# Kernel tuning notes

Hardware: AMD Instinct MI355X
Metric: run time of the kernel (lower is better)

Reference implementation:

```python
import jax, jax.numpy as jnp
import numpy as np

B, S, D, H, DFF = 4, 2048, 1024, 16, 4096
DK = D // H


def layer_norm(x, g, b, eps=1e-5):
    mu = jnp.mean(x, axis=-1, keepdims=True)
    var = jnp.mean((x - mu) ** 2, axis=-1, keepdims=True)
    return (x - mu) / jnp.sqrt(var + eps) * g + b


def setup_inputs() -> dict:
    key = jax.random.key(0)
    ks = jax.random.split(key, 16)
    w = lambda k, shape: jax.random.normal(k, shape, jnp.float32) * 0.02
    return {
        "x": jax.random.normal(ks[0], (B, S, D), jnp.float32),
        "w_q": w(ks[1], (D, D)), "b_q": jnp.zeros((D,), jnp.float32),
        "w_k": w(ks[2], (D, D)), "b_k": jnp.zeros((D,), jnp.float32),
        "w_v": w(ks[3], (D, D)), "b_v": jnp.zeros((D,), jnp.float32),
        "w_o": w(ks[4], (D, D)), "b_o": jnp.zeros((D,), jnp.float32),
        "w_g": w(ks[5], (D, H)), "b_g": jnp.zeros((H,), jnp.float32),
        "w1": w(ks[6], (D, DFF)), "b1": jnp.zeros((DFF,), jnp.float32),
        "w2": w(ks[7], (DFF, D)), "b2": jnp.zeros((D,), jnp.float32),
        "g1": jnp.ones((D,), jnp.float32), "beta1": jnp.zeros((D,), jnp.float32),
        "g2": jnp.ones((D,), jnp.float32), "beta2": jnp.zeros((D,), jnp.float32),
        "mask": jnp.ones((B, 1, 1, S), jnp.int32),
    }


def reference(x, w_q, b_q, w_k, b_k, w_v, b_v, w_o, b_o, w_g, b_g,
              w1, b1, w2, b2, g1, beta1, g2, beta2, mask):
    b, s, d = x.shape
    scale = DK ** -0.5
    # QKV projections -> [B,H,S,DK]
    q = (x @ w_q + b_q).reshape(b, s, H, DK).transpose(0, 2, 1, 3)
    k = (x @ w_k + b_k).reshape(b, s, H, DK).transpose(0, 2, 1, 3)
    v = (x @ w_v + b_v).reshape(b, s, H, DK).transpose(0, 2, 1, 3)
    scores = jnp.einsum("bhqd,bhkd->bhqk", q, k) * scale  # [B,H,S,S]
    scores = jnp.where(mask == 0, jnp.float32(-1e9), scores)
    attn = jax.nn.softmax(scores, axis=-1)
    # per-(token, head) sigmoid gate applied post-softmax
    gate = jax.nn.sigmoid(x @ w_g + b_g)            # [B,S,H]
    attn = attn * gate.transpose(0, 2, 1)[..., None]  # [B,H,S,1]
    ctx = jnp.einsum("bhqk,bhkd->bhqd", attn, v)
    ctx = ctx.transpose(0, 2, 1, 3).reshape(b, s, d)
    attn_out = ctx @ w_o + b_o
    x1 = layer_norm(x + attn_out, g1, beta1)
    ff = jax.nn.gelu(x1 @ w1 + b1, approximate=False) @ w2 + b2
    return layer_norm(x1 + ff, g2, beta2)
```

## Files before the change

kernel.cpp:

```cpp
#include <hip/hip_runtime.h>
#include <hip/hip_bf16.h>
#include <cstdint>


typedef __bf16 bf16x8 __attribute__((ext_vector_type(8)));
typedef float  f32x4  __attribute__((ext_vector_type(4)));

__device__ __forceinline__ uint16_t f2bf_bits(float f) {
    __hip_bfloat16 h = __float2bfloat16(f);
    return __builtin_bit_cast(uint16_t, h);
}

#define GLOAD16(ldsb, gp) __builtin_amdgcn_global_load_lds( \
    (const __attribute__((address_space(1))) void*)(gp),    \
    (__attribute__((address_space(3))) void*)(ldsb), 16, 0, 0)

__global__ __launch_bounds__(256) void cast_bf16_kernel(
    const float* __restrict__ in, __hip_bfloat16* __restrict__ out, size_t n4)
{
    size_t i = (size_t)blockIdx.x * blockDim.x + threadIdx.x;
    if (i >= n4) return;
    float4 v = ((const float4*)in)[i];
    ushort4 o;
    o.x = f2bf_bits(v.x); o.y = f2bf_bits(v.y);
    o.z = f2bf_bits(v.z); o.w = f2bf_bits(v.w);
    ((ushort4*)out)[i] = o;
}

__global__ __launch_bounds__(256) void transpose_cast_kernel(
    const float* __restrict__ in, __hip_bfloat16* __restrict__ out, int K, int N)
{
    __shared__ float t[32][33];
    int n0 = blockIdx.x * 32, k0 = blockIdx.y * 32;
    int tx = threadIdx.x, ty = threadIdx.y;
#pragma unroll
    for (int i = 0; i < 4; ++i)
        t[ty + i * 8][tx] = in[(size_t)(k0 + ty + i * 8) * N + n0 + tx];
    __syncthreads();
#pragma unroll
    for (int i = 0; i < 4; ++i)
        out[(size_t)(n0 + ty + i * 8) * K + k0 + tx] = __float2bfloat16(t[tx][ty + i * 8]);
}

__global__ __launch_bounds__(256) void gate_kernel(
    const float* __restrict__ x, const float* __restrict__ wg,
    const float* __restrict__ bg, float* __restrict__ gate)
{
    int tid = threadIdx.x, lane = tid & 63, wid = tid >> 6;
    int row = blockIdx.x * 4 + wid;
    const float* xr = x + (size_t)row * 1024;
    float acc[16];
#pragma unroll
    for (int hh = 0; hh < 16; ++hh) acc[hh] = 0.0f;
    for (int k = lane; k < 1024; k += 64) {
        float xv = xr[k];
        const float* wr = wg + (size_t)k * 16;
#pragma unroll
        for (int hh = 0; hh < 16; ++hh) acc[hh] = fmaf(xv, wr[hh], acc[hh]);
    }
#pragma unroll
    for (int hh = 0; hh < 16; ++hh) {
#pragma unroll
        for (int d = 1; d < 64; d <<= 1) acc[hh] += __shfl_xor(acc[hh], d);
    }
    if (lane < 16) {
        float v = 0.0f;
#pragma unroll
        for (int hh = 0; hh < 16; ++hh)
            if (lane == hh) v = acc[hh] + bg[hh];
        gate[(size_t)row * 16 + lane] = 1.0f / (1.0f + __expf(-v));
    }
}

__global__ __launch_bounds__(256) void ln_kernel(
    const float* __restrict__ A, const float* __restrict__ Bx,
    const float* __restrict__ g, const float* __restrict__ beta,
    float* __restrict__ outf, __hip_bfloat16* __restrict__ outb)
{
    int row = blockIdx.x, tid = threadIdx.x;
    const float4* a4 = (const float4*)(A  + (size_t)row * 1024);
    const float4* b4 = (const float4*)(Bx + (size_t)row * 1024);
    float4 va = a4[tid], vb = b4[tid];
    float x0 = va.x + vb.x, x1 = va.y + vb.y, x2 = va.z + vb.z, x3 = va.w + vb.w;
    float s  = x0 + x1 + x2 + x3;
    float sq = x0 * x0 + x1 * x1 + x2 * x2 + x3 * x3;
#pragma unroll
    for (int d = 1; d < 64; d <<= 1) { s += __shfl_xor(s, d); sq += __shfl_xor(sq, d); }
    __shared__ float ss[4], ssq[4];
    int wid = tid >> 6, lane = tid & 63;
    if (lane == 0) { ss[wid] = s; ssq[wid] = sq; }
    __syncthreads();
    s  = ss[0] + ss[1] + ss[2] + ss[3];
    sq = ssq[0] + ssq[1] + ssq[2] + ssq[3];
    float mean = s * (1.0f / 1024.0f);
    float var  = sq * (1.0f / 1024.0f) - mean * mean;
    float rstd = rsqrtf(var + 1e-5f);
    float4 gv = ((const float4*)g)[tid], bv = ((const float4*)beta)[tid];
    float y0 = (x0 - mean) * rstd * gv.x + bv.x;
    float y1 = (x1 - mean) * rstd * gv.y + bv.y;
    float y2 = (x2 - mean) * rstd * gv.z + bv.z;
    float y3 = (x3 - mean) * rstd * gv.w + bv.w;
    float4 o; o.x = y0; o.y = y1; o.z = y2; o.w = y3;
    ((float4*)(outf + (size_t)row * 1024))[tid] = o;
    if (outb) {
        ushort4 ob;
        ob.x = f2bf_bits(y0); ob.y = f2bf_bits(y1);
        ob.z = f2bf_bits(y2); ob.w = f2bf_bits(y3);
        ((ushort4*)(outb + (size_t)row * 1024))[tid] = ob;
    }
}

template<int EPI>
__global__ __launch_bounds__(256, 2) void gemm128(
    const __hip_bfloat16* __restrict__ A,
    const __hip_bfloat16* __restrict__ BT,
    const float* __restrict__ bias,
    void* __restrict__ Cout, int M, int N, int K)
{
    __shared__ __align__(16) __hip_bfloat16 As[128 * 64];
    __shared__ __align__(16) __hip_bfloat16 Bs[128 * 64];
    const int tid = threadIdx.x, lane = tid & 63, wid = tid >> 6;
    const int bx = blockIdx.x, by = blockIdx.y;
    const int wr = wid >> 1, wc = wid & 1;

    f32x4 acc[4][4];
#pragma unroll
    for (int i = 0; i < 4; ++i)
#pragma unroll
        for (int j = 0; j < 4; ++j) acc[i][j] = (f32x4){0.f, 0.f, 0.f, 0.f};

    const char* Abase = (const char*)A  + (size_t)(by * 128) * K * 2;
    const char* Bbase = (const char*)BT + (size_t)(bx * 128) * K * 2;
    char* AsB = (char*)As; char* BsB = (char*)Bs;
    const int laneRow = lane >> 3;
    const int laneCol = (lane & 7) * 16;

    for (int ks = 0; ks < K; ks += 64) {
#pragma unroll
        for (int j = 0; j < 4; ++j) {
            int r = j * 32 + wid * 8 + laneRow;
            size_t goff = (size_t)r * K * 2 + (size_t)ks * 2 + laneCol;
            GLOAD16(AsB + j * 4096 + wid * 1024, Abase + goff);
            GLOAD16(BsB + j * 4096 + wid * 1024, Bbase + goff);
        }
        __syncthreads();
#pragma unroll
        for (int kk = 0; kk < 2; ++kk) {
            const int kob = (kk * 32 + (lane >> 4) * 8) * 2;
            bf16x8 a[4], b[4];
#pragma unroll
            for (int mt = 0; mt < 4; ++mt)
                a[mt] = *(const bf16x8*)(AsB + (wr * 64 + mt * 16 + (lane & 15)) * 128 + kob);
#pragma unroll
            for (int nt = 0; nt < 4; ++nt)
                b[nt] = *(const bf16x8*)(BsB + (wc * 64 + nt * 16 + (lane & 15)) * 128 + kob);
#pragma unroll
            for (int mt = 0; mt < 4; ++mt)
#pragma unroll
                for (int nt = 0; nt < 4; ++nt)
                    acc[mt][nt] = __builtin_amdgcn_mfma_f32_16x16x32_bf16(
                        a[mt], b[nt], acc[mt][nt], 0, 0, 0);
        }
        __syncthreads();
    }

    const int m0 = by * 128 + wr * 64;
    const int n0 = bx * 128 + wc * 64;
#pragma unroll
    for (int mt = 0; mt < 4; ++mt) {
#pragma unroll
        for (int nt = 0; nt < 4; ++nt) {
            int n = n0 + nt * 16 + (lane & 15);
            float bv = bias[n];
#pragma unroll
            for (int j = 0; j < 4; ++j) {
                int m = m0 + mt * 16 + (lane >> 4) * 4 + j;
                float v = acc[mt][nt][j] + bv;
                ((float*)Cout)[(size_t)m * N + n] = v;
            }
        }
    }
}

template<int EPI>
__global__ __launch_bounds__(512, 2) void gemm256(
    const __hip_bfloat16* __restrict__ A,
    const __hip_bfloat16* __restrict__ BT,
    const float* __restrict__ bias0,
    const float* __restrict__ bias1,
    const float* __restrict__ bias2,
    __hip_bfloat16* __restrict__ out0,
    __hip_bfloat16* __restrict__ out1,
    __hip_bfloat16* __restrict__ out2,
    int M, int N, int K)
{
    __shared__ __align__(16) char lds_[131072];
    const int tid = threadIdx.x;
    const int lane = tid & 63;
    const int l15 = lane & 15;
    const int wid = tid >> 6;
    const int wm = wid >> 2, wn = wid & 3;

    const int NBX = N >> 8;
    const int cpx = ((M >> 8) * NBX) >> 3;
    const int nl = ((int)blockIdx.x & 7) * cpx + ((int)blockIdx.x >> 3);
    const int by = nl / NBX, bx = nl % NBX;

    const char* Abase = (const char*)A  + (size_t)(by * 256) * K * 2;
    const char* Bbase = (const char*)BT + (size_t)(bx * 256) * K * 2;

    const int srow = tid >> 3;
    const int ssw  = ((tid & 7) ^ (srow & 7)) * 16;

    f32x4 acc[8][4];
#pragma unroll
    for (int i = 0; i < 8; ++i)
#pragma unroll
        for (int j = 0; j < 4; ++j) acc[i][j] = (f32x4){0.f, 0.f, 0.f, 0.f};

    auto stageA = [&](int d, int c, int ks) {
        const char* src = Abase + ((size_t)(c * 64 + srow) * K + ks) * 2 + ssw;
        GLOAD16(lds_ + d * 65536 + c * 8192 + wid * 1024, src);
    };
    auto stageB = [&](int d, int c, int ks) {
        const char* src = Bbase + ((size_t)(c * 64 + srow) * K + ks) * 2 + ssw;
        GLOAD16(lds_ + d * 65536 + 32768 + c * 8192 + wid * 1024, src);
    };

    const int NT = K >> 6;
    stageB(0, 0, 0); stageB(0, 1, 0); stageB(0, 2, 0); stageB(0, 3, 0);
    stageA(0, 0, 0); stageA(0, 2, 0); stageA(0, 1, 0); stageA(0, 3, 0);
    asm volatile("s_waitcnt vmcnt(0)" ::: "memory");
    __builtin_amdgcn_s_barrier();

    for (int t = 0; t < NT; ++t) {
        const int cur = t & 1, nxt = cur ^ 1;
        const int ksn = (t + 1) << 6;
        const bool st = (t + 1 < NT);
        const char* ldsA = lds_ + cur * 65536;
        const char* ldsB = ldsA + 32768;

        bf16x8 bfr[4][2];
#pragma unroll
        for (int p = 0; p < 4; ++p) {
            if (p == 0) {
#pragma unroll
                for (int nf = 0; nf < 4; ++nf) {
                    const int br = wn * 64 + nf * 16 + l15;
#pragma unroll
                    for (int kk = 0; kk < 2; ++kk) {
                        const int kb = kk * 64 + (lane >> 4) * 16;
                        bfr[nf][kk] = *(const bf16x8*)(ldsB + (br >> 6) * 8192 +
                            (br & 63) * 128 + (kb ^ ((br & 7) << 4)));
                    }
                }
            }
            bf16x8 afr[2][2];
#pragma unroll
            for (int mi = 0; mi < 2; ++mi) {
                const int ar = wm * 128 + (2 * p + mi) * 16 + l15;
#pragma unroll
                for (int kk = 0; kk < 2; ++kk) {
                    const int kb = kk * 64 + (lane >> 4) * 16;
                    afr[mi][kk] = *(const bf16x8*)(ldsA + (ar >> 6) * 8192 +
                        (ar & 63) * 128 + (kb ^ ((ar & 7) << 4)));
                }
            }
            if (st) {
                if      (p == 0) { stageB(nxt, 0, ksn); stageB(nxt, 1, ksn); }
                else if (p == 1) { stageB(nxt, 2, ksn); stageB(nxt, 3, ksn); }
                else if (p == 2) { stageA(nxt, 0, ksn); stageA(nxt, 2, ksn); }
                else             { stageA(nxt, 1, ksn); stageA(nxt, 3, ksn); }
            }
            __builtin_amdgcn_s_barrier();
            __builtin_amdgcn_s_setprio(1);
#pragma unroll
            for (int mi = 0; mi < 2; ++mi)
#pragma unroll
                for (int nf = 0; nf < 4; ++nf)
#pragma unroll
                    for (int kk = 0; kk < 2; ++kk)
                        acc[2 * p + mi][nf] = __builtin_amdgcn_mfma_f32_16x16x32_bf16(
                            afr[mi][kk], bfr[nf][kk], acc[2 * p + mi][nf], 0, 0, 0);
            __builtin_amdgcn_s_setprio(0);
            if (p == 1) asm volatile("s_waitcnt vmcnt(4)" ::: "memory");
            if (p == 3) asm volatile("s_waitcnt vmcnt(2)" ::: "memory");
            __builtin_amdgcn_s_barrier();
        }
    }

    const int nbase = bx * 256 + wn * 64;
    const int mbase = by * 256 + wm * 128;
    if constexpr (EPI == 5) {
        const int reg = nbase >> 10;
        const float* bias = (reg == 0) ? bias0 : (reg == 1) ? bias1 : bias2;
#pragma unroll
        for (int mf = 0; mf < 8; ++mf) {
#pragma unroll
            for (int nf = 0; nf < 4; ++nf) {
                const int n = nbase + nf * 16 + l15;
                const int nn = n & 1023, h = nn >> 6, dk = nn & 63;
                const float bv = bias[nn];
#pragma unroll
                for (int j = 0; j < 4; ++j) {
                    const int m = mbase + mf * 16 + (lane >> 4) * 4 + j;
                    const int b = m >> 11, s = m & 2047;
                    const float v = acc[mf][nf][j] + bv;
                    if (reg == 0)
                        out0[((((size_t)b * 16 + h) * 2048 + s) << 6) + dk] =
                            __float2bfloat16(v * 0.125f);
                    else if (reg == 1)
                        out1[((((size_t)b * 16 + h) * 2048 + s) << 6) + dk] =
                            __float2bfloat16(v);
                    else
                        out2[(((size_t)b * 16 + h) * 64 + dk) * 2048 + s] =
                            __float2bfloat16(v);
                }
            }
        }
    } else {
#pragma unroll
        for (int mf = 0; mf < 8; ++mf) {
#pragma unroll
            for (int nf = 0; nf < 4; ++nf) {
                const int n = nbase + nf * 16 + l15;
                const float bv = bias0[n];
#pragma unroll
                for (int j = 0; j < 4; ++j) {
                    const int m = mbase + mf * 16 + (lane >> 4) * 4 + j;
                    const float v = acc[mf][nf][j] + bv;
                    const float ge = 0.5f * v * (1.0f + erff(v * 0.70710678118654752f));
                    out0[(size_t)m * N + n] = __float2bfloat16(ge);
                }
            }
        }
    }
}

__global__ __launch_bounds__(256, 2) void attn_kernel(
    const __hip_bfloat16* __restrict__ Q,
    const __hip_bfloat16* __restrict__ Kg,
    const __hip_bfloat16* __restrict__ Vt,
    const float* __restrict__ gate,
    const int* __restrict__ mask,
    __hip_bfloat16* __restrict__ ctx)
{
    __shared__ __align__(16) __hip_bfloat16 Ks[64 * 64];
    __shared__ __align__(16) __hip_bfloat16 Vs[64 * 64];
    __shared__ __align__(16) __hip_bfloat16 Ps[4][16 * 64];
    const int tid = threadIdx.x, lane = tid & 63, wid = tid >> 6;

    int lin = blockIdx.x;
    int nl  = (lin & 7) * 256 + (lin >> 3);
    const int bh = nl >> 5, qt = nl & 31;
    const int b = bh >> 4, h = bh & 15;
    const int q0 = qt * 64 + wid * 16;

    bf16x8 aq[2];
    const __hip_bfloat16* Qbase = Q + ((size_t)bh * 2048 + q0) * 64;
#pragma unroll
    for (int kk = 0; kk < 2; ++kk)
        aq[kk] = *(const bf16x8*)(Qbase + (lane & 15) * 64 + kk * 32 + (lane >> 4) * 8);

    f32x4 octx[4];
#pragma unroll
    for (int dt = 0; dt < 4; ++dt) octx[dt] = (f32x4){0.f, 0.f, 0.f, 0.f};
    float m_run[4], l_run[4];
#pragma unroll
    for (int r = 0; r < 4; ++r) { m_run[r] = -1e30f; l_run[r] = 0.0f; }

    const char* Kbase = (const char*)(Kg + (size_t)bh * 2048 * 64);
    const char* Vbase = (const char*)(Vt + (size_t)bh * 64 * 2048);
    char* KsB = (char*)Ks; char* VsB = (char*)Vs;
    char* PsB = (char*)&Ps[wid][0];

    const int srow = (lane >> 3);
    const int schunk = lane & 7;

    for (int kv0 = 0; kv0 < 2048; kv0 += 64) {
#pragma unroll
        for (int j = 0; j < 2; ++j) {
            int off = j * 4096 + wid * 1024;
            int row = j * 32 + wid * 8 + srow;
            int sc  = (schunk ^ (row & 7)) * 16;
            GLOAD16(KsB + off, Kbase + (size_t)(kv0 + row) * 128 + sc);
            GLOAD16(VsB + off, Vbase + (size_t)row * 4096 + (size_t)kv0 * 2 + sc);
        }
        __syncthreads();

        f32x4 sfr[4];
#pragma unroll
        for (int ct = 0; ct < 4; ++ct) sfr[ct] = (f32x4){0.f, 0.f, 0.f, 0.f};
#pragma unroll
        for (int kk = 0; kk < 2; ++kk) {
            const int kob = (kk * 32 + (lane >> 4) * 8) * 2;
#pragma unroll
            for (int ct = 0; ct < 4; ++ct) {
                int krow = ct * 16 + (lane & 15);
                bf16x8 bk = *(const bf16x8*)(KsB + ((krow * 128 + kob) ^ ((krow & 7) << 4)));
                sfr[ct] = __builtin_amdgcn_mfma_f32_16x16x32_bf16(aq[kk], bk, sfr[ct], 0, 0, 0);
            }
        }
#pragma unroll
        for (int ct = 0; ct < 4; ++ct) {
            int kvi = kv0 + ct * 16 + (lane & 15);
            if (mask[b * 2048 + kvi] == 0) {
                sfr[ct][0] = -1e9f; sfr[ct][1] = -1e9f;
                sfr[ct][2] = -1e9f; sfr[ct][3] = -1e9f;
            }
        }
#pragma unroll
        for (int r = 0; r < 4; ++r) {
            float mx = fmaxf(fmaxf(sfr[0][r], sfr[1][r]), fmaxf(sfr[2][r], sfr[3][r]));
            mx = fmaxf(mx, __shfl_xor(mx, 1));
            mx = fmaxf(mx, __shfl_xor(mx, 2));
            mx = fmaxf(mx, __shfl_xor(mx, 4));
            mx = fmaxf(mx, __shfl_xor(mx, 8));
            float mn = fmaxf(m_run[r], mx);
            float c  = __expf(m_run[r] - mn);
            m_run[r] = mn;
            float s = 0.0f;
#pragma unroll
            for (int ct = 0; ct < 4; ++ct) {
                float p = __expf(sfr[ct][r] - mn);
                sfr[ct][r] = p;
                s += p;
            }
            s += __shfl_xor(s, 1); s += __shfl_xor(s, 2);
            s += __shfl_xor(s, 4); s += __shfl_xor(s, 8);
            l_run[r] = l_run[r] * c + s;
#pragma unroll
            for (int dt = 0; dt < 4; ++dt) octx[dt][r] *= c;
        }
#pragma unroll
        for (int ct = 0; ct < 4; ++ct) {
#pragma unroll
            for (int r = 0; r < 4; ++r) {
                int qr = (lane >> 4) * 4 + r;
                int byteoff = (qr * 128 + (ct * 16 + (lane & 15)) * 2) ^ ((qr & 7) << 4);
                *(__hip_bfloat16*)(PsB + byteoff) = __float2bfloat16(sfr[ct][r]);
            }
        }
#pragma unroll
        for (int kk = 0; kk < 2; ++kk) {
            const int kb = kk * 32 + (lane >> 4) * 8;
            int pbyte = ((lane & 15) * 128 + kb * 2) ^ (((lane & 15) & 7) << 4);
            bf16x8 ap = *(const bf16x8*)(PsB + pbyte);
#pragma unroll
            for (int dt = 0; dt < 4; ++dt) {
                int vrow = dt * 16 + (lane & 15);
                bf16x8 bvv = *(const bf16x8*)(VsB + ((vrow * 128 + kb * 2) ^ ((vrow & 7) << 4)));
                octx[dt] = __builtin_amdgcn_mfma_f32_16x16x32_bf16(ap, bvv, octx[dt], 0, 0, 0);
            }
        }
        __syncthreads();
    }

#pragma unroll
    for (int r = 0; r < 4; ++r) {
        int qg = q0 + (lane >> 4) * 4 + r;
        size_t rowm = (size_t)b * 2048 + qg;
        float gv = gate[rowm * 16 + h];
        float inv = gv / l_run[r];
#pragma unroll
        for (int dt = 0; dt < 4; ++dt)
            ctx[rowm * 1024 + h * 64 + dt * 16 + (lane & 15)] =
                __float2bfloat16(octx[dt][r] * inv);
    }
}

extern "C" void kernel_launch(void* const* d_in, const int* in_sizes, int n_in,
                              void* d_out, int out_size, void* d_ws, size_t ws_size,
                              hipStream_t stream)
{
    const float* x    = (const float*)d_in[0];
    const float* w_q  = (const float*)d_in[1];
    const float* b_q  = (const float*)d_in[2];
    const float* w_k  = (const float*)d_in[3];
    const float* b_k  = (const float*)d_in[4];
    const float* w_v  = (const float*)d_in[5];
    const float* b_v  = (const float*)d_in[6];
    const float* w_o  = (const float*)d_in[7];
    const float* b_o  = (const float*)d_in[8];
    const float* w_g  = (const float*)d_in[9];
    const float* b_g  = (const float*)d_in[10];
    const float* w1   = (const float*)d_in[11];
    const float* b1   = (const float*)d_in[12];
    const float* w2   = (const float*)d_in[13];
    const float* b2   = (const float*)d_in[14];
    const float* g1   = (const float*)d_in[15];
    const float* be1  = (const float*)d_in[16];
    const float* g2   = (const float*)d_in[17];
    const float* be2  = (const float*)d_in[18];
    const int*   mask = (const int*)d_in[19];

    char* ws = (char*)d_ws;
    size_t off = 0;
    auto alloc = [&](size_t bytes) -> char* {
        char* p = ws + off; off += (bytes + 255) & ~(size_t)255; return p;
    };

    char* regionA = alloc(67108864);
    __hip_bfloat16* xb   = (__hip_bfloat16*)regionA;
    __hip_bfloat16* qb   = (__hip_bfloat16*)(regionA + 16777216);
    __hip_bfloat16* kb   = (__hip_bfloat16*)(regionA + 33554432);
    __hip_bfloat16* vb   = (__hip_bfloat16*)(regionA + 50331648);
    __hip_bfloat16* hbuf = (__hip_bfloat16*)regionA;

    __hip_bfloat16* wqT = (__hip_bfloat16*)alloc(2097152);
    __hip_bfloat16* wkT = (__hip_bfloat16*)alloc(2097152);
    __hip_bfloat16* wvT = (__hip_bfloat16*)alloc(2097152);
    __hip_bfloat16* woT = (__hip_bfloat16*)alloc(2097152);
    __hip_bfloat16* w1T = (__hip_bfloat16*)alloc(8388608);
    __hip_bfloat16* w2T = (__hip_bfloat16*)alloc(8388608);
    float* gate       = (float*)alloc(524288);
    __hip_bfloat16* ctx = (__hip_bfloat16*)alloc(16777216);
    float* attn_out   = (float*)alloc(33554432);
    float* x1f        = (float*)alloc(33554432);
    __hip_bfloat16* x1b = (__hip_bfloat16*)alloc(16777216);

    dim3 tb(32, 8);
    cast_bf16_kernel<<<8192, 256, 0, stream>>>(x, xb, 2097152);
    transpose_cast_kernel<<<dim3(32, 32),  tb, 0, stream>>>(w_q, wqT, 1024, 1024);
    transpose_cast_kernel<<<dim3(32, 32),  tb, 0, stream>>>(w_k, wkT, 1024, 1024);
    transpose_cast_kernel<<<dim3(32, 32),  tb, 0, stream>>>(w_v, wvT, 1024, 1024);
    transpose_cast_kernel<<<dim3(32, 32),  tb, 0, stream>>>(w_o, woT, 1024, 1024);
    transpose_cast_kernel<<<dim3(128, 32), tb, 0, stream>>>(w1, w1T, 1024, 4096);
    transpose_cast_kernel<<<dim3(32, 128), tb, 0, stream>>>(w2, w2T, 4096, 1024);
    gate_kernel<<<2048, 256, 0, stream>>>(x, w_g, b_g, gate);

    gemm256<5><<<384, 512, 0, stream>>>(xb, wqT, b_q, b_k, b_v, qb, kb, vb,
                                        8192, 3072, 1024);

    attn_kernel<<<2048, 256, 0, stream>>>(qb, kb, vb, gate, mask, ctx);

    gemm128<0><<<dim3(8, 64), 256, 0, stream>>>(ctx, woT, b_o, attn_out, 8192, 1024, 1024);
    ln_kernel<<<8192, 256, 0, stream>>>(x, attn_out, g1, be1, x1f, x1b);
    gemm256<6><<<512, 512, 0, stream>>>(x1b, w1T, b1, nullptr, nullptr,
                                        hbuf, nullptr, nullptr, 8192, 4096, 1024);
    gemm128<0><<<dim3(8, 64), 256, 0, stream>>>(hbuf, w2T, b2, attn_out, 8192, 1024, 4096);
    ln_kernel<<<8192, 256, 0, stream>>>(x1f, attn_out, g2, be2, (float*)d_out, nullptr);
}
```

Before: 776.3 us.

## Use wave-wide lazy max rescaling in flash attention softmax

Replaces the per-row online-softmax max and sum reductions with one wave-wide running max. The max is only rescaled when some lane exceeds it by more than a threshold, and the row sums are deferred to a single shuffle reduction at the end. The mask load is hoisted before the barrier and applied as an additive term, and s_setprio brackets the MFMA sections. This cuts shuffle and exp work in the inner loop. The risks are precision loss when rows in a wave have very different maxima (possible underflow) and exponent growth of up to e^8 in bf16 P.

```diff
diff --git a/kernel.cpp b/kernel.cpp
--- a/kernel.cpp
+++ b/kernel.cpp
@@ -365,9 +365,8 @@
     f32x4 octx[4];
 #pragma unroll
     for (int dt = 0; dt < 4; ++dt) octx[dt] = (f32x4){0.f, 0.f, 0.f, 0.f};
-    float m_run[4], l_run[4];
-#pragma unroll
-    for (int r = 0; r < 4; ++r) { m_run[r] = -1e30f; l_run[r] = 0.0f; }
+    float l_part[4] = {0.f, 0.f, 0.f, 0.f};
+    float m_cur = 0.0f;
 
     const char* Kbase = (const char*)(Kg + (size_t)bh * 2048 * 64);
     const char* Vbase = (const char*)(Vt + (size_t)bh * 64 * 2048);
@@ -386,11 +385,18 @@
             GLOAD16(KsB + off, Kbase + (size_t)(kv0 + row) * 128 + sc);
             GLOAD16(VsB + off, Vbase + (size_t)row * 4096 + (size_t)kv0 * 2 + sc);
         }
+        float madd[4];
+#pragma unroll
+        for (int ct = 0; ct < 4; ++ct) {
+            int kvi = kv0 + ct * 16 + (lane & 15);
+            madd[ct] = (mask[b * 2048 + kvi] == 0) ? -1e9f : 0.0f;
+        }
         __syncthreads();
 
         f32x4 sfr[4];
 #pragma unroll
         for (int ct = 0; ct < 4; ++ct) sfr[ct] = (f32x4){0.f, 0.f, 0.f, 0.f};
+        __builtin_amdgcn_s_setprio(1);
 #pragma unroll
         for (int kk = 0; kk < 2; ++kk) {
             const int kob = (kk * 32 + (lane >> 4) * 8) * 2;
@@ -401,46 +407,51 @@
                 sfr[ct] = __builtin_amdgcn_mfma_f32_16x16x32_bf16(aq[kk], bk, sfr[ct], 0, 0, 0);
             }
         }
+        __builtin_amdgcn_s_setprio(0);
 #pragma unroll
         for (int ct = 0; ct < 4; ++ct) {
-            int kvi = kv0 + ct * 16 + (lane & 15);
-            if (mask[b * 2048 + kvi] == 0) {
-                sfr[ct][0] = -1e9f; sfr[ct][1] = -1e9f;
-                sfr[ct][2] = -1e9f; sfr[ct][3] = -1e9f;
-            }
-        }
-#pragma unroll
-        for (int r = 0; r < 4; ++r) {
-            float mx = fmaxf(fmaxf(sfr[0][r], sfr[1][r]), fmaxf(sfr[2][r], sfr[3][r]));
-            mx = fmaxf(mx, __shfl_xor(mx, 1));
-            mx = fmaxf(mx, __shfl_xor(mx, 2));
-            mx = fmaxf(mx, __shfl_xor(mx, 4));
-            mx = fmaxf(mx, __shfl_xor(mx, 8));
-            float mn = fmaxf(m_run[r], mx);
-            float c  = __expf(m_run[r] - mn);
-            m_run[r] = mn;
-            float s = 0.0f;
-#pragma unroll
-            for (int ct = 0; ct < 4; ++ct) {
-                float p = __expf(sfr[ct][r] - mn);
-                sfr[ct][r] = p;
-                s += p;
-            }
-            s += __shfl_xor(s, 1); s += __shfl_xor(s, 2);
-            s += __shfl_xor(s, 4); s += __shfl_xor(s, 8);
-            l_run[r] = l_run[r] * c + s;
-#pragma unroll
-            for (int dt = 0; dt < 4; ++dt) octx[dt][r] *= c;
-        }
+#pragma unroll
+            for (int r = 0; r < 4; ++r) sfr[ct][r] += madd[ct];
+        }
+
+        float mlane = sfr[0][0];
+#pragma unroll
+        for (int ct = 0; ct < 4; ++ct)
+#pragma unroll
+            for (int r = 0; r < 4; ++r) mlane = fmaxf(mlane, sfr[ct][r]);
+
+        if (kv0 == 0) {
+            float wm = mlane;
+#pragma unroll
+            for (int d = 1; d < 64; d <<= 1) wm = fmaxf(wm, __shfl_xor(wm, d));
+            m_cur = wm;
+        } else if (!__all(mlane <= m_cur + 8.0f)) {
+            float wm = mlane;
+#pragma unroll
+            for (int d = 1; d < 64; d <<= 1) wm = fmaxf(wm, __shfl_xor(wm, d));
+            wm = fmaxf(wm, m_cur);
+            float c = __expf(m_cur - wm);
+            m_cur = wm;
+#pragma unroll
+            for (int dt = 0; dt < 4; ++dt)
+#pragma unroll
+                for (int r = 0; r < 4; ++r) octx[dt][r] *= c;
+#pragma unroll
+            for (int r = 0; r < 4; ++r) l_part[r] *= c;
+        }
+
 #pragma unroll
         for (int ct = 0; ct < 4; ++ct) {
 #pragma unroll
             for (int r = 0; r < 4; ++r) {
+                float p = __expf(sfr[ct][r] - m_cur);
+                l_part[r] += p;
                 int qr = (lane >> 4) * 4 + r;
                 int byteoff = (qr * 128 + (ct * 16 + (lane & 15)) * 2) ^ ((qr & 7) << 4);
-                *(__hip_bfloat16*)(PsB + byteoff) = __float2bfloat16(sfr[ct][r]);
-            }
-        }
+                *(__hip_bfloat16*)(PsB + byteoff) = __float2bfloat16(p);
+            }
+        }
+        __builtin_amdgcn_s_setprio(1);
 #pragma unroll
         for (int kk = 0; kk < 2; ++kk) {
             const int kb = kk * 32 + (lane >> 4) * 8;
@@ -453,7 +464,16 @@
                 octx[dt] = __builtin_amdgcn_mfma_f32_16x16x32_bf16(ap, bvv, octx[dt], 0, 0, 0);
             }
         }
+        __builtin_amdgcn_s_setprio(0);
         __syncthreads();
+    }
+
+#pragma unroll
+    for (int r = 0; r < 4; ++r) {
+        float s = l_part[r];
+        s += __shfl_xor(s, 1); s += __shfl_xor(s, 2);
+        s += __shfl_xor(s, 4); s += __shfl_xor(s, 8);
+        l_part[r] = s;
     }
 
 #pragma unroll
@@ -461,7 +481,7 @@
         int qg = q0 + (lane >> 4) * 4 + r;
         size_t rowm = (size_t)b * 2048 + qg;
         float gv = gate[rowm * 16 + h];
-        float inv = gv / l_run[r];
+        float inv = gv / l_part[r];
 #pragma unroll
         for (int dt = 0; dt < 4; ++dt)
             ctx[rowm * 1024 + h * 64 + dt * 16 + (lane & 15)] =
```

Result: faster. 666.9 us (-14.1%).
